# Optimization experiments

Hardware: AMD Instinct MI355X
Metric: run time of the kernel (lower is better)

Reference implementation:

```python
import jax, jax.numpy as jnp
import numpy as np

H = W = 200
A = 9
N = H * W * A  # 360000 anchors
PRE_NMS = 6000   # test mode
POST_NMS = 300
MIN_SIZE = 16.0 / 1000.0
IOU_THR = 0.7


def _conv(x, w, b, pad):
    y = jax.lax.conv_general_dilated(x, w, (1, 1), pad,
                                     dimension_numbers=("NCHW", "OIHW", "NCHW"))
    return y + b[None, :, None, None]


def _nms_keep(boxes, valid, thr):
    # boxes: [PRE_NMS,4] sorted by descending score; valid: [PRE_NMS] bool
    x1, y1, x2, y2 = boxes[:, 0], boxes[:, 1], boxes[:, 2], boxes[:, 3]
    areas = (x2 - x1) * (y2 - y1)
    idx = jnp.arange(boxes.shape[0])

    def body(i, keep):
        xx1 = jnp.maximum(x1[i], x1)
        yy1 = jnp.maximum(y1[i], y1)
        xx2 = jnp.minimum(x2[i], x2)
        yy2 = jnp.minimum(y2[i], y2)
        inter = jnp.clip(xx2 - xx1, 0.0) * jnp.clip(yy2 - yy1, 0.0)
        iou = inter / (areas[i] + areas - inter + 1e-12)
        suppress = (iou > thr) & (idx > i) & keep[i]
        return keep & ~suppress

    return jax.lax.fori_loop(0, boxes.shape[0], body, valid)


def setup_inputs():
    key = jax.random.key(0)
    ks = jax.random.split(key, 6)
    features = jax.random.normal(ks[0], (1, 512, H, W), dtype=jnp.float32)
    # valid anchor boxes (xyxy, normalized)
    c = jax.random.uniform(ks[1], (N, 2), dtype=jnp.float32)
    wh = jax.random.uniform(ks[2], (N, 2), dtype=jnp.float32, minval=0.02, maxval=0.4)
    anchor = jnp.clip(jnp.concatenate([c - wh / 2, c + wh / 2], axis=1), 0.0, 1.0)
    w1 = 0.01 * jax.random.normal(ks[3], (512, 512, 3, 3), dtype=jnp.float32)
    b1 = jnp.zeros((512,), jnp.float32)
    wc = 0.01 * jax.random.normal(ks[4], (2 * A, 512, 1, 1), dtype=jnp.float32)
    bc = jnp.zeros((2 * A,), jnp.float32)
    wl = 0.01 * jax.random.normal(ks[5], (4 * A, 512, 1, 1), dtype=jnp.float32)
    bl = jnp.zeros((4 * A,), jnp.float32)
    return {"features": features, "anchor": anchor,
            "w1": w1, "b1": b1, "wc": wc, "bc": bc, "wl": wl, "bl": bl}


def reference(features, anchor, w1, b1, wc, bc, wl, bl):
    x = jax.nn.relu(_conv(features, w1, b1, ((1, 1), (1, 1))))
    pred_cls = _conv(x, wc, bc, ((0, 0), (0, 0)))
    pred_loc = _conv(x, wl, bl, ((0, 0), (0, 0)))
    pred_cls = jnp.transpose(pred_cls, (0, 2, 3, 1)).reshape(1, -1, 2)  # [1,N,2]
    pred_loc = jnp.transpose(pred_loc, (0, 2, 3, 1)).reshape(1, -1, 4)  # [1,N,4]

    loc = pred_loc[0]
    cls = pred_cls[0]
    # xy_to_cxcy
    a_cxcy = jnp.concatenate([(anchor[:, 2:] + anchor[:, :2]) / 2.0,
                              anchor[:, 2:] - anchor[:, :2]], axis=1)
    # decode
    cxcy = loc[:, :2] * a_cxcy[:, 2:] + a_cxcy[:, :2]
    wh = jnp.exp(loc[:, 2:]) * a_cxcy[:, 2:]
    # cxcy_to_xy + clamp
    roi = jnp.clip(jnp.concatenate([cxcy - wh / 2.0, cxcy + wh / 2.0], axis=1), 0.0, 1.0)

    scores = jax.nn.softmax(cls, axis=-1)[:, 1]
    ws = roi[:, 2] - roi[:, 0]
    hs = roi[:, 3] - roi[:, 1]
    valid = (hs >= MIN_SIZE) & (ws >= MIN_SIZE)
    scores = jnp.where(valid, scores, -1.0)  # filtered boxes sort last

    top_scores, top_idx = jax.lax.top_k(scores, PRE_NMS)
    boxes = roi[top_idx]                      # [PRE_NMS,4]
    valid_top = top_scores >= 0.0

    keep = jax.lax.stop_gradient(_nms_keep(boxes, valid_top, IOU_THR))
    # first POST_NMS kept boxes, in score order; pad with zeros (fixed shape)
    priority = jnp.where(keep, jnp.arange(PRE_NMS), PRE_NMS)
    order = jnp.argsort(priority)[:POST_NMS]
    rois = jnp.where((priority[order] < PRE_NMS)[:, None], boxes[order], 0.0)  # [300,4]
    return pred_cls, pred_loc, rois
```

## Files before the change

### kernel.cpp

```cpp
#include <hip/hip_runtime.h>

typedef unsigned long long u64;
typedef unsigned int u32;
typedef unsigned short ushort_t;

#define HH 200
#define WW 200
#define HWP 40000
#define NANCH 360000
#define PRE 6000
#define POST 300
#define NW 94
#define NBINS 16384
#define KCAP 8192
#define LSTRIDE 40

typedef __attribute__((ext_vector_type(8))) _Float16 f16x8;
typedef __attribute__((ext_vector_type(4))) float f32x4;

static constexpr size_t X_F    = 0;
static constexpr size_t X_CNT  = 512ULL*HWP + 64;
static constexpr size_t W1B_F  = X_F + X_CNT;
static constexpr size_t WT64_F = W1B_F + 4608ULL*512;
static constexpr size_t B64_F  = WT64_F + 512ULL*64;
static constexpr size_t SC_F   = B64_F + 64;
static constexpr size_t ROI_F  = SC_F + NANCH;
static constexpr size_t BOX_F  = ROI_F + 4ULL*NANCH;
static constexpr size_t FEND_F = BOX_F + 6016ULL*4;
static constexpr size_t HIST_B = ((FEND_F*4 + 255)/256)*256;
static constexpr size_t CTRL_B = HIST_B + NBINS*4;
static constexpr size_t KEY_B  = CTRL_B + 256;
static constexpr size_t SORT_B = KEY_B + (size_t)KCAP*8;
static constexpr size_t VALW_B = SORT_B + 6016ULL*8;
static constexpr size_t MASK_B = ((VALW_B + NW*8 + 255)/256)*256;
static constexpr size_t OFFT_B = MASK_B + (size_t)PRE*NW*8;
static constexpr size_t WS_END = OFFT_B + 4608ULL*4;

__device__ __forceinline__ u32 fsort(float f) {
  u32 u = __float_as_uint(f);
  return (u & 0x80000000u) ? ~u : (u | 0x80000000u);
}
__device__ __forceinline__ int bucket_of(float s) {
  int b = (int)((s + 1.0f) * 8191.0f);
  return b < 0 ? 0 : (b > 16383 ? 16383 : b);
}
__device__ __forceinline__ ushort_t h_bits(_Float16 h) {
  union { _Float16 h; ushort_t u; } c; c.h = h; return c.u;
}

__global__ void pack_w1b(const float* __restrict__ w1, ushort_t* __restrict__ p12) {
  int idx = blockIdx.x*256 + threadIdx.x;
  if (idx >= 512*4608) return;
  int och = idx / 4608, k = idx - (idx/4608)*4608;
  float f = w1[idx];
  _Float16 h1 = (_Float16)f;
  float r = f - (float)h1;
  _Float16 h2 = (_Float16)(r * 2048.0f);
  int z = och >> 7, oz = och & 127;
  int wnb = oz >> 6, j = (oz >> 4) & 3, lm = oz & 15;
  int s = k >> 5, kk = k & 31, lg = kk >> 3, e = kk & 7;
  int lane = lg*16 + lm;
  size_t base = (((size_t)z*144 + s)*2 + wnb)*4 + j;
  p12[base*1024 +       lane*8 + e] = h_bits(h1);
  p12[base*1024 + 512 + lane*8 + e] = h_bits(h2);
}

__global__ void init_offtab(u32* __restrict__ offTab) {
  int k = blockIdx.x*256 + threadIdx.x;
  if (k >= 4608) return;
  int ci = k/9, tap = k - ci*9;
  int dy = tap/3 - 1, dx = tap - (tap/3)*3 - 1;
  int off = ci*HWP + dy*200 + dx;
  offTab[k] = ((u32)(off + 256) << 4) | (u32)tap;
}

__global__ void pack_wcl(const float* __restrict__ wc, const float* __restrict__ bc,
                         const float* __restrict__ wl, const float* __restrict__ bl,
                         float* __restrict__ wt, float* __restrict__ b64) {
  int idx = blockIdx.x*256 + threadIdx.x;
  if (idx < 512*64) {
    int ci = idx >> 6, o = idx & 63;
    float v = 0.f;
    if (o < 18) v = wc[o*512 + ci];
    else if (o < 54) v = wl[(o-18)*512 + ci];
    wt[idx] = v;
  } else if (idx < 512*64 + 64) {
    int o = idx - 512*64;
    float v = 0.f;
    if (o < 18) v = bc[o]; else if (o < 54) v = bl[o-18];
    b64[o] = v;
  }
}

__global__ __launch_bounds__(256, 2) void conv3x3_mfma(const float* __restrict__ feat,
    const ushort_t* __restrict__ p12,
    const u32* __restrict__ offTab,
    const float* __restrict__ b1, float* __restrict__ xout) {
  __shared__ ushort_t A1[128*LSTRIDE], A2[128*LSTRIDE];
  const int t = threadIdx.x;
  const int x0 = blockIdx.x*16, y0 = blockIdx.y*8;
  const int zi = blockIdx.z;
  const int ob = zi*128;
  const int m  = t & 127;
  const int hU = __builtin_amdgcn_readfirstlane(t >> 7);
  const int myrow = m >> 4, mxcol = m & 15;
  const int py = y0 + myrow, px = x0 + mxcol;
  const int pixoff = py*200 + px;

  u32 vmask9 = 0;
  #pragma unroll
  for (int tap = 0; tap < 9; ++tap) {
    int dy = tap/3 - 1, dx = tap - (tap/3)*3 - 1;
    if ((unsigned)(py + dy) < 200u && (unsigned)(px + dx) < 200u) vmask9 |= (1u << tap);
  }

  f32x4 accM[4][4], accC[4][4];
  #pragma unroll
  for (int i = 0; i < 4; ++i)
    #pragma unroll
    for (int j = 0; j < 4; ++j) {
      accM[i][j] = (f32x4){0.f, 0.f, 0.f, 0.f};
      accC[i][j] = (f32x4){0.f, 0.f, 0.f, 0.f};
    }

  const int wave = t >> 6, lane = t & 63;
  const int wm = (wave & 1)*64, wnb = wave >> 1;
  const int lm = lane & 15, lg = lane >> 4;
  const u32* offp = offTab + 16*hU;

  for (int s = 0; s < 144; ++s) {
    f16x8 fb1[4], fb2[4];
    {
      const ushort_t* pb12 = p12 + ((((size_t)zi*144 + s)*2 + wnb)*4096) + lane*8;
      #pragma unroll
      for (int j = 0; j < 4; ++j) {
        fb1[j] = *(const f16x8*)(pb12 + j*1024);
        fb2[j] = *(const f16x8*)(pb12 + j*1024 + 512);
      }
    }
    {
      const u32* op = offp + s*32;
      u32 q1[8], q2[8];
      #pragma unroll
      for (int j2 = 0; j2 < 8; ++j2) {
        float fv[2];
        #pragma unroll
        for (int e = 0; e < 2; ++e) {
          u32 ent = op[2*j2 + e];
          int soff = (int)(ent >> 4) - 256;
          u32 tap  = ent & 15u;
          bool ok  = ((vmask9 >> tap) & 1u) != 0;
          int voff = ok ? (soff + pixoff) : 0;
          float f = feat[voff];
          fv[e] = ok ? f : 0.f;
        }
        _Float16 h0 = (_Float16)fv[0], h1v = (_Float16)fv[1];
        float r0 = fv[0] - (float)h0;
        float r1 = fv[1] - (float)h1v;
        _Float16 c0 = (_Float16)(r0 * 2048.0f), c1 = (_Float16)(r1 * 2048.0f);
        q1[j2] = (u32)h_bits(h0) | ((u32)h_bits(h1v) << 16);
        q2[j2] = (u32)h_bits(c0) | ((u32)h_bits(c1) << 16);
      }
      *(uint4*)&A1[m*LSTRIDE + 16*hU    ] = make_uint4(q1[0], q1[1], q1[2], q1[3]);
      *(uint4*)&A1[m*LSTRIDE + 16*hU + 8] = make_uint4(q1[4], q1[5], q1[6], q1[7]);
      *(uint4*)&A2[m*LSTRIDE + 16*hU    ] = make_uint4(q2[0], q2[1], q2[2], q2[3]);
      *(uint4*)&A2[m*LSTRIDE + 16*hU + 8] = make_uint4(q2[4], q2[5], q2[6], q2[7]);
    }
    __syncthreads();
    f16x8 fa1[4], fa2[4];
    #pragma unroll
    for (int i = 0; i < 4; ++i) {
      int ra = (wm + i*16 + lm)*LSTRIDE + lg*8;
      fa1[i] = *(const f16x8*)&A1[ra];
      fa2[i] = *(const f16x8*)&A2[ra];
    }
    #pragma unroll
    for (int i = 0; i < 4; ++i)
      #pragma unroll
      for (int j = 0; j < 4; ++j) {
        accM[i][j] = __builtin_amdgcn_mfma_f32_16x16x32_f16(fa1[i], fb1[j], accM[i][j], 0, 0, 0);
        accC[i][j] = __builtin_amdgcn_mfma_f32_16x16x32_f16(fa1[i], fb2[j], accC[i][j], 0, 0, 0);
        accC[i][j] = __builtin_amdgcn_mfma_f32_16x16x32_f16(fa2[i], fb1[j], accC[i][j], 0, 0, 0);
      }
    __syncthreads();
  }

  #pragma unroll
  for (int i = 0; i < 4; ++i) {
    int prow = wm + i*16 + lg*4;
    #pragma unroll
    for (int j = 0; j < 4; ++j) {
      int o = ob + wnb*64 + j*16 + lm;
      float bias = b1[o];
      #pragma unroll
      for (int r = 0; r < 4; ++r) {
        int p  = prow + r;
        int yy = y0 + (p >> 4), xx = x0 + (p & 15);
        if (xx < WW) {
          float v = accM[i][j][r] + accC[i][j][r] * 4.8828125e-4f + bias;
          xout[(size_t)o*HWP + yy*200 + xx] = fmaxf(v, 0.f);
        }
      }
    }
  }
}

__global__ __launch_bounds__(256, 4) void conv1x1(const float* __restrict__ x,
                                                  const float* __restrict__ wt,
                                                  const float* __restrict__ bias,
                                                  float* __restrict__ out) {
  __shared__ float Xs[16*128];
  __shared__ float Ws[16*64];
  const int t = threadIdx.x;
  const int m0 = blockIdx.x*128;
  float acc[32];
  #pragma unroll
  for (int i = 0; i < 32; ++i) acc[i] = 0.f;
  const int mb = t & 15, nb = t >> 4;
  const int mm = t & 127, hh = t >> 7;
  const int nn = t & 63,  h2 = t >> 6;

  for (int kb = 0; kb < 512; kb += 16) {
    #pragma unroll
    for (int j = 0; j < 8; ++j) {
      int kk = hh + 2*j;
      Xs[kk*128 + mm] = x[(size_t)(kb+kk)*HWP + m0 + mm];
    }
    #pragma unroll
    for (int j = 0; j < 4; ++j) {
      int kk = h2 + 4*j;
      Ws[kk*64 + nn] = wt[(size_t)(kb+kk)*64 + nn];
    }
    __syncthreads();
    #pragma unroll
    for (int kk = 0; kk < 16; ++kk) {
      float av[8], bv[4];
      *(float4*)&av[0] = *(const float4*)&Xs[kk*128 + mb*8];
      *(float4*)&av[4] = *(const float4*)&Xs[kk*128 + mb*8 + 4];
      *(float4*)&bv[0] = *(const float4*)&Ws[kk*64 + nb*4];
      #pragma unroll
      for (int i = 0; i < 8; ++i)
        #pragma unroll
        for (int jj = 0; jj < 4; ++jj)
          acc[i*4+jj] = fmaf(av[i], bv[jj], acc[i*4+jj]);
    }
    __syncthreads();
  }

  #pragma unroll
  for (int jj = 0; jj < 4; ++jj) {
    int o = nb*4 + jj;
    float bv = bias[o];
    #pragma unroll
    for (int i = 0; i < 8; ++i) {
      int mm2 = m0 + mb*8 + i;
      if (mm2 < HWP) {
        float v = acc[i*4+jj] + bv;
        if (o < 18)       out[(size_t)mm2*18 + o] = v;
        else if (o < 54)  out[720000 + (size_t)mm2*36 + (o-18)] = v;
      }
    }
  }
}

__global__ void decode(const float* __restrict__ dout, const float* __restrict__ anchor,
                       float* __restrict__ scores, float4* __restrict__ roi, u32* __restrict__ hist) {
  int n = blockIdx.x*256 + threadIdx.x;
  if (n >= NANCH) return;
  int mq = n / 9;
  int a  = n - mq*9;
  float c0 = dout[(size_t)mq*18 + 2*a];
  float c1 = dout[(size_t)mq*18 + 2*a + 1];
  float score = 1.0f / (1.0f + expf(c0 - c1));
  const float* lp = dout + 720000 + (size_t)mq*36 + 4*a;
  float l0 = lp[0], l1 = lp[1], l2 = lp[2], l3 = lp[3];
  float4 an = ((const float4*)anchor)[n];
  float aw = an.z - an.x, ah = an.w - an.y;
  float acx = (an.x + an.z)*0.5f, acy = (an.y + an.w)*0.5f;
  float cx = l0*aw + acx, cy = l1*ah + acy;
  float bw = expf(l2)*aw, bh = expf(l3)*ah;
  float x1 = fminf(fmaxf(cx - bw*0.5f, 0.f), 1.f);
  float y1 = fminf(fmaxf(cy - bh*0.5f, 0.f), 1.f);
  float x2 = fminf(fmaxf(cx + bw*0.5f, 0.f), 1.f);
  float y2 = fminf(fmaxf(cy + bh*0.5f, 0.f), 1.f);
  bool valid = ((y2 - y1) >= 0.016f) && ((x2 - x1) >= 0.016f);
  float sc = valid ? score : -1.0f;
  scores[n] = sc;
  roi[n] = make_float4(x1, y1, x2, y2);
  atomicAdd(&hist[bucket_of(sc)], 1u);
}

__global__ void scan_hist(const u32* __restrict__ hist, u32* __restrict__ ctrl) {
  __shared__ u32 seg[256];
  int t = threadIdx.x;
  u32 s = 0;
  for (int b = 0; b < 64; ++b) s += hist[t*64 + b];
  seg[t] = s;
  __syncthreads();
  if (t == 0) {
    u32 cum = 0; int B = 0;
    for (int sg = 255; sg >= 0; --sg) {
      if (cum + seg[sg] >= PRE) {
        for (int b = sg*64 + 63; b >= sg*64; --b) {
          cum += hist[b];
          if (cum >= PRE) { B = b; break; }
        }
        break;
      }
      cum += seg[sg];
    }
    ctrl[1] = (u32)B;
  }
}

__global__ void compact(const float* __restrict__ scores, u32* __restrict__ ctrl, u64* __restrict__ keybuf) {
  int n = blockIdx.x*256 + threadIdx.x;
  if (n >= NANCH) return;
  float s = scores[n];
  int B = (int)ctrl[1];
  if (bucket_of(s) >= B) {
    u32 pos = atomicAdd(&ctrl[0], 1u);
    if (pos < KCAP) {
      keybuf[pos] = ((u64)fsort(s) << 32) | (u64)(0xFFFFFFFFu - (u32)n);
    }
  }
}

__global__ __launch_bounds__(1024) void sortk(const u64* __restrict__ keybuf, const u32* __restrict__ ctrl,
                                              u64* __restrict__ sorted) {
  __shared__ u64 s[KCAP];
  int t = threadIdx.x;
  u32 cnt = ctrl[0]; if (cnt > KCAP) cnt = KCAP;
  for (int i = t; i < KCAP; i += 1024) s[i] = (i < (int)cnt) ? keybuf[i] : 0ULL;
  __syncthreads();
  for (int size = 2; size <= KCAP; size <<= 1) {
    for (int stride = size >> 1; stride > 0; stride >>= 1) {
      for (int w = t; w < KCAP/2; w += 1024) {
        int lo = ((w & ~(stride-1)) << 1) | (w & (stride-1));
        int hi = lo + stride;
        bool desc = ((lo & size) == 0);
        u64 a = s[lo], b = s[hi];
        if ((a < b) == desc) { s[lo] = b; s[hi] = a; }
      }
      __syncthreads();
    }
  }
  for (int i = t; i < 6016; i += 1024) sorted[i] = s[i];
}

__global__ void gather_topk(const u64* __restrict__ sorted, const float4* __restrict__ roi,
                            float4* __restrict__ boxes, u64* __restrict__ validw) {
  int i = blockIdx.x*64 + threadIdx.x;
  bool valid = false;
  float4 b = make_float4(0.f, 0.f, 0.f, 0.f);
  if (i < PRE) {
    u64 k = sorted[i];
    if (k) {
      u32 n = 0xFFFFFFFFu - (u32)(k & 0xFFFFFFFFu);
      if (n < NANCH) { b = roi[n]; valid = (k >> 63) != 0; }
    }
  }
  boxes[i] = b;
  u64 bal = __ballot(valid);
  if (threadIdx.x == 0) validw[blockIdx.x] = bal;
}

__global__ void nms_mask(const float4* __restrict__ boxes, u64* __restrict__ mask) {
  int bi = blockIdx.y, bj = blockIdx.x;
  int t = threadIdx.x;
  int i = bi*64 + t;
  if (bj < bi) {
    if (i < PRE) mask[(size_t)i*NW + bj] = 0ULL;
    return;
  }
  __shared__ float4 cb[64];
  int j0 = bj*64;
  cb[t] = boxes[j0 + t];
  __syncthreads();
  if (i >= PRE) return;
  float4 b = boxes[i];
  float area_i = (b.z - b.x) * (b.w - b.y);
  u64 bits = 0;
  #pragma unroll 4
  for (int jj = 0; jj < 64; ++jj) {
    int j = j0 + jj;
    float4 c = cb[jj];
    float xx1 = fmaxf(b.x, c.x), yy1 = fmaxf(b.y, c.y);
    float xx2 = fminf(b.z, c.z), yy2 = fminf(b.w, c.w);
    float inter = fmaxf(xx2 - xx1, 0.f) * fmaxf(yy2 - yy1, 0.f);
    float area_j = (c.z - c.x) * (c.w - c.y);
    float iou = inter / (area_i + area_j - inter + 1e-12f);
    if (iou > 0.7f && j > i) bits |= (1ULL << jj);
  }
  mask[(size_t)i*NW + bj] = bits;
}

__global__ void nms_scan(const u64* __restrict__ mask, const u64* __restrict__ validw,
                         const float* __restrict__ boxes, float* __restrict__ rois) {
  int lane = threadIdx.x;
  u64 r0 = ~validw[lane];
  u64 r1 = (lane < NW-64) ? ~validw[64 + lane] : ~0ULL;
  int kept = 0;
  u64 m0 = mask[lane];
  u64 m1 = (lane < NW-64) ? mask[64 + lane] : 0ULL;
  for (int i = 0; i < PRE; ++i) {
    int wi = i >> 6;
    u64 w0 = __shfl(r0, wi & 63);
    u64 w1 = __shfl(r1, wi & 63);
    u64 wv = (wi < 64) ? w0 : w1;
    if (!((wv >> (i & 63)) & 1ULL)) {
      if (lane < 4) rois[kept*4 + lane] = boxes[(size_t)i*4 + lane];
      kept++;
      if (kept >= POST) break;
      r0 |= m0;
      if (lane < NW-64) r1 |= m1;
    }
    if (i + 1 < PRE) {
      m0 = mask[(size_t)(i+1)*NW + lane];
      m1 = (lane < NW-64) ? mask[(size_t)(i+1)*NW + 64 + lane] : 0ULL;
    }
  }
}

extern "C" void kernel_launch(void* const* d_in, const int* in_sizes, int n_in,
                              void* d_out, int out_size, void* d_ws, size_t ws_size,
                              hipStream_t stream) {
  const float* feat   = (const float*)d_in[0];
  const float* anchor = (const float*)d_in[1];
  const float* w1     = (const float*)d_in[2];
  const float* b1     = (const float*)d_in[3];
  const float* wc     = (const float*)d_in[4];
  const float* bc     = (const float*)d_in[5];
  const float* wl     = (const float*)d_in[6];
  const float* bl     = (const float*)d_in[7];
  float* out = (float*)d_out;
  char*  ws  = (char*)d_ws;
  float* wsf = (float*)d_ws;

  if (ws_size < WS_END) return;

  float*    x      = wsf + X_F;
  ushort_t* p12    = (ushort_t*)(wsf + W1B_F);
  float*    wt64   = wsf + WT64_F;
  float*    b64    = wsf + B64_F;
  float*    scores = wsf + SC_F;
  float4*   roi    = (float4*)(wsf + ROI_F);
  float4*   boxes  = (float4*)(wsf + BOX_F);
  u32* hist   = (u32*)(ws + HIST_B);
  u32* ctrl   = (u32*)(ws + CTRL_B);
  u64* keybuf = (u64*)(ws + KEY_B);
  u64* sorted = (u64*)(ws + SORT_B);
  u64* validw = (u64*)(ws + VALW_B);
  u64* mask   = (u64*)(ws + MASK_B);
  u32* offTab = (u32*)(ws + OFFT_B);

  hipMemsetAsync(ws + HIST_B, 0, NBINS*4 + 256, stream);
  hipMemsetAsync(out + 2160000, 0, POST*4*sizeof(float), stream);

  pack_w1b<<<9216, 256, 0, stream>>>(w1, p12);
  init_offtab<<<18, 256, 0, stream>>>(offTab);
  pack_wcl<<<129, 256, 0, stream>>>(wc, bc, wl, bl, wt64, b64);
  conv3x3_mfma<<<dim3(13, 25, 4), 256, 0, stream>>>(feat, p12, offTab, b1, x);
  conv1x1<<<313, 256, 0, stream>>>(x, wt64, b64, out);
  decode<<<1407, 256, 0, stream>>>(out, anchor, scores, roi, hist);
  scan_hist<<<1, 256, 0, stream>>>(hist, ctrl);
  compact<<<1407, 256, 0, stream>>>(scores, ctrl, keybuf);
  sortk<<<1, 1024, 0, stream>>>(keybuf, ctrl, sorted);
  gather_topk<<<NW, 64, 0, stream>>>(sorted, roi, boxes, validw);
  nms_mask<<<dim3(NW, NW), 64, 0, stream>>>(boxes, mask);
  nms_scan<<<1, 64, 0, stream>>>(mask, validw, (const float*)boxes, out + 2160000);
}
```

Measured before the change: 1.460 ms.

## Stage halo input tile per channel chunk and reuse across nine taps

The 3x3 conv stops gathering an im2col tile from global memory for every K-step. It now loads a 10x18 halo tile for 32 input channels into shared memory once, splits it into fp16 hi/lo parts, and reads all nine tap shifts from that tile. Weights are repacked so K is ordered by channel chunk and then tap, which removes the offset table kernel. This cuts redundant global loads, conversion work and barriers by about nine times. The cost is possible LDS bank conflicts from the 32-wide channel stride and idle threads on the x<18 guard.

Result: slower. 1.674 ms (+14.6%).

```diff
diff --git a/kernel.cpp b/kernel.cpp
--- a/kernel.cpp
+++ b/kernel.cpp
@@ -13,7 +13,6 @@
 #define NW 94
 #define NBINS 16384
 #define KCAP 8192
-#define LSTRIDE 40
 
 typedef __attribute__((ext_vector_type(8))) _Float16 f16x8;
 typedef __attribute__((ext_vector_type(4))) float f32x4;
@@ -33,8 +32,7 @@
 static constexpr size_t SORT_B = KEY_B + (size_t)KCAP*8;
 static constexpr size_t VALW_B = SORT_B + 6016ULL*8;
 static constexpr size_t MASK_B = ((VALW_B + NW*8 + 255)/256)*256;
-static constexpr size_t OFFT_B = MASK_B + (size_t)PRE*NW*8;
-static constexpr size_t WS_END = OFFT_B + 4608ULL*4;
+static constexpr size_t WS_END = MASK_B + (size_t)PRE*NW*8;
 
 __device__ __forceinline__ u32 fsort(float f) {
   u32 u = __float_as_uint(f);
@@ -56,22 +54,16 @@
   _Float16 h1 = (_Float16)f;
   float r = f - (float)h1;
   _Float16 h2 = (_Float16)(r * 2048.0f);
+  int ci = k / 9, tap = k - ci*9;
+  int chunk = ci >> 5, cil = ci & 31;
+  int s = chunk*9 + tap;
   int z = och >> 7, oz = och & 127;
-  int wnb = oz >> 6, j = (oz >> 4) & 3, lm = oz & 15;
-  int s = k >> 5, kk = k & 31, lg = kk >> 3, e = kk & 7;
-  int lane = lg*16 + lm;
+  int wnb = oz >> 6, j = (oz >> 4) & 3, lmm = oz & 15;
+  int lg = cil >> 3, e = cil & 7;
+  int lane = lg*16 + lmm;
   size_t base = (((size_t)z*144 + s)*2 + wnb)*4 + j;
   p12[base*1024 +       lane*8 + e] = h_bits(h1);
   p12[base*1024 + 512 + lane*8 + e] = h_bits(h2);
-}
-
-__global__ void init_offtab(u32* __restrict__ offTab) {
-  int k = blockIdx.x*256 + threadIdx.x;
-  if (k >= 4608) return;
-  int ci = k/9, tap = k - ci*9;
-  int dy = tap/3 - 1, dx = tap - (tap/3)*3 - 1;
-  int off = ci*HWP + dy*200 + dx;
-  offTab[k] = ((u32)(off + 256) << 4) | (u32)tap;
 }
 
 __global__ void pack_wcl(const float* __restrict__ wc, const float* __restrict__ bc,
@@ -94,25 +86,21 @@
 
 __global__ __launch_bounds__(256, 2) void conv3x3_mfma(const float* __restrict__ feat,
     const ushort_t* __restrict__ p12,
-    const u32* __restrict__ offTab,
     const float* __restrict__ b1, float* __restrict__ xout) {
-  __shared__ ushort_t A1[128*LSTRIDE], A2[128*LSTRIDE];
+  __shared__ ushort_t H1[10*18*32], H2[10*18*32];
   const int t = threadIdx.x;
   const int x0 = blockIdx.x*16, y0 = blockIdx.y*8;
   const int zi = blockIdx.z;
   const int ob = zi*128;
-  const int m  = t & 127;
-  const int hU = __builtin_amdgcn_readfirstlane(t >> 7);
-  const int myrow = m >> 4, mxcol = m & 15;
-  const int py = y0 + myrow, px = x0 + mxcol;
-  const int pixoff = py*200 + px;
-
-  u32 vmask9 = 0;
-  #pragma unroll
-  for (int tap = 0; tap < 9; ++tap) {
-    int dy = tap/3 - 1, dx = tap - (tap/3)*3 - 1;
-    if ((unsigned)(py + dy) < 200u && (unsigned)(px + dx) < 200u) vmask9 |= (1u << tap);
-  }
+
+  const int wave = t >> 6, lane = t & 63;
+  const int wm = (wave & 1)*64, wnb = wave >> 1;
+  const int lm = lane & 15, lg = lane >> 4;
+  const int lyb = wm >> 4;
+  const int fragoff = lm*32 + lg*8;
+
+  const int sci = t >> 3;
+  const int sxo = t & 7;
 
   f32x4 accM[4][4], accC[4][4];
   #pragma unroll
@@ -123,66 +111,62 @@
       accC[i][j] = (f32x4){0.f, 0.f, 0.f, 0.f};
     }
 
-  const int wave = t >> 6, lane = t & 63;
-  const int wm = (wave & 1)*64, wnb = wave >> 1;
-  const int lm = lane & 15, lg = lane >> 4;
-  const u32* offp = offTab + 16*hU;
-
-  for (int s = 0; s < 144; ++s) {
-    f16x8 fb1[4], fb2[4];
-    {
-      const ushort_t* pb12 = p12 + ((((size_t)zi*144 + s)*2 + wnb)*4096) + lane*8;
+  const ushort_t* pb = p12 + (size_t)zi*1179648 + (size_t)wnb*4096 + lane*8;
+  const float* fbc = feat + (size_t)sci*HWP;
+
+  for (int c = 0; c < 16; ++c) {
+    __syncthreads();
+    #pragma unroll
+    for (int y = 0; y < 10; ++y) {
+      int gy = y0 + y - 1;
+      bool yok = (unsigned)gy < 200u;
+      int rowoff = gy*200 + x0 - 1;
+      #pragma unroll
+      for (int k = 0; k < 3; ++k) {
+        int x = sxo + 8*k;
+        int gx = x0 + x - 1;
+        bool ok = yok && (x < 18) && ((unsigned)gx < 200u);
+        int off = ok ? (rowoff + x) : 0;
+        float f = fbc[off];
+        f = ok ? f : 0.f;
+        _Float16 h1 = (_Float16)f;
+        float r = f - (float)h1;
+        _Float16 h2 = (_Float16)(r * 2048.0f);
+        if (x < 18) {
+          int a = (y*18 + x)*32 + sci;
+          H1[a] = h_bits(h1);
+          H2[a] = h_bits(h2);
+        }
+      }
+    }
+    __syncthreads();
+    #pragma unroll
+    for (int tap = 0; tap < 9; ++tap) {
+      const int dy = tap/3, dx = tap - (tap/3)*3;
+      f16x8 fb1[4], fb2[4];
       #pragma unroll
       for (int j = 0; j < 4; ++j) {
-        fb1[j] = *(const f16x8*)(pb12 + j*1024);
-        fb2[j] = *(const f16x8*)(pb12 + j*1024 + 512);
-      }
-    }
-    {
-      const u32* op = offp + s*32;
-      u32 q1[8], q2[8];
-      #pragma unroll
-      for (int j2 = 0; j2 < 8; ++j2) {
-        float fv[2];
+        fb1[j] = *(const f16x8*)(pb + j*1024);
+        fb2[j] = *(const f16x8*)(pb + j*1024 + 512);
+      }
+      f16x8 fa1[4], fa2[4];
+      #pragma unroll
+      for (int i = 0; i < 4; ++i) {
+        int addr = (lyb + i + dy)*576 + dx*32 + fragoff;
+        fa1[i] = *(const f16x8*)&H1[addr];
+        fa2[i] = *(const f16x8*)&H2[addr];
+      }
+      #pragma unroll
+      for (int i = 0; i < 4; ++i)
         #pragma unroll
-        for (int e = 0; e < 2; ++e) {
-          u32 ent = op[2*j2 + e];
-          int soff = (int)(ent >> 4) - 256;
-          u32 tap  = ent & 15u;
-          bool ok  = ((vmask9 >> tap) & 1u) != 0;
-          int voff = ok ? (soff + pixoff) : 0;
-          float f = feat[voff];
-          fv[e] = ok ? f : 0.f;
+        for (int j = 0; j < 4; ++j) {
+          accM[i][j] = __builtin_amdgcn_mfma_f32_16x16x32_f16(fa1[i], fb1[j], accM[i][j], 0, 0, 0);
+          accC[i][j] = __builtin_amdgcn_mfma_f32_16x16x32_f16(fa1[i], fb2[j], accC[i][j], 0, 0, 0);
+          accC[i][j] = __builtin_amdgcn_mfma_f32_16x16x32_f16(fa2[i], fb1[j], accC[i][j], 0, 0, 0);
         }
-        _Float16 h0 = (_Float16)fv[0], h1v = (_Float16)fv[1];
-        float r0 = fv[0] - (float)h0;
-        float r1 = fv[1] - (float)h1v;
-        _Float16 c0 = (_Float16)(r0 * 2048.0f), c1 = (_Float16)(r1 * 2048.0f);
-        q1[j2] = (u32)h_bits(h0) | ((u32)h_bits(h1v) << 16);
-        q2[j2] = (u32)h_bits(c0) | ((u32)h_bits(c1) << 16);
-      }
-      *(uint4*)&A1[m*LSTRIDE + 16*hU    ] = make_uint4(q1[0], q1[1], q1[2], q1[3]);
-      *(uint4*)&A1[m*LSTRIDE + 16*hU + 8] = make_uint4(q1[4], q1[5], q1[6], q1[7]);
-      *(uint4*)&A2[m*LSTRIDE + 16*hU    ] = make_uint4(q2[0], q2[1], q2[2], q2[3]);
-      *(uint4*)&A2[m*LSTRIDE + 16*hU + 8] = make_uint4(q2[4], q2[5], q2[6], q2[7]);
-    }
-    __syncthreads();
-    f16x8 fa1[4], fa2[4];
-    #pragma unroll
-    for (int i = 0; i < 4; ++i) {
-      int ra = (wm + i*16 + lm)*LSTRIDE + lg*8;
-      fa1[i] = *(const f16x8*)&A1[ra];
-      fa2[i] = *(const f16x8*)&A2[ra];
-    }
-    #pragma unroll
-    for (int i = 0; i < 4; ++i)
-      #pragma unroll
-      for (int j = 0; j < 4; ++j) {
-        accM[i][j] = __builtin_amdgcn_mfma_f32_16x16x32_f16(fa1[i], fb1[j], accM[i][j], 0, 0, 0);
-        accC[i][j] = __builtin_amdgcn_mfma_f32_16x16x32_f16(fa1[i], fb2[j], accC[i][j], 0, 0, 0);
-        accC[i][j] = __builtin_amdgcn_mfma_f32_16x16x32_f16(fa2[i], fb1[j], accC[i][j], 0, 0, 0);
-      }
-    __syncthreads();
+      pb += 8192;
+    }
+    fbc += 32*HWP;
   }
 
   #pragma unroll
@@ -452,15 +436,13 @@
   u64* sorted = (u64*)(ws + SORT_B);
   u64* validw = (u64*)(ws + VALW_B);
   u64* mask   = (u64*)(ws + MASK_B);
-  u32* offTab = (u32*)(ws + OFFT_B);
 
   hipMemsetAsync(ws + HIST_B, 0, NBINS*4 + 256, stream);
   hipMemsetAsync(out + 2160000, 0, POST*4*sizeof(float), stream);
 
   pack_w1b<<<9216, 256, 0, stream>>>(w1, p12);
-  init_offtab<<<18, 256, 0, stream>>>(offTab);
   pack_wcl<<<129, 256, 0, stream>>>(wc, bc, wl, bl, wt64, b64);
-  conv3x3_mfma<<<dim3(13, 25, 4), 256, 0, stream>>>(feat, p12, offTab, b1, x);
+  conv3x3_mfma<<<dim3(13, 25, 4), 256, 0, stream>>>(feat, p12, b1, x);
   conv1x1<<<313, 256, 0, stream>>>(x, wt64, b64, out);
   decode<<<1407, 256, 0, stream>>>(out, anchor, scores, roi, hist);
   scan_hist<<<1, 256, 0, stream>>>(hist, ctrl);
```
